# Kernel tuning notes

Measured on AMD Instinct MI355X. Metric: run time of the kernel, lower is better.

The kernel has to match this reference:

```python
import jax, jax.numpy as jnp
import numpy as np

NUM_SEGMENTS = 512
N = 200000
D = 256


def setup_inputs() -> dict:
    key = jax.random.key(0)
    k = jax.random.split(key, 6)
    x = jax.random.normal(k[0], (N, D), dtype=jnp.float32)
    batch = jnp.sort(jax.random.randint(k[1], (N,), 0, NUM_SEGMENTS))
    batch = batch.at[-1].set(NUM_SEGMENTS - 1)  # ensure batch.max()+1 == NUM_SEGMENTS
    W1 = jax.random.normal(k[2], (D, D // 2), dtype=jnp.float32) * (1.0 / np.sqrt(D))
    b1 = jax.random.normal(k[3], (D // 2,), dtype=jnp.float32) * 0.01
    W2 = jax.random.normal(k[4], (D // 2, 1), dtype=jnp.float32) * (1.0 / np.sqrt(D // 2))
    b2 = jax.random.normal(k[5], (1,), dtype=jnp.float32) * 0.01
    return {"x": x, "batch": batch, "W1": W1, "b1": b1, "W2": W2, "b2": b2}


def reference(x, batch, W1, b1, W2, b2):
    # attention MLP: Linear -> Tanh -> Linear -> [N, 1]
    scores = (jnp.tanh(x @ W1 + b1) @ W2 + b2)[:, 0]  # [N]
    # segment softmax (numerically stable): subtract per-segment max
    smax = jax.ops.segment_max(scores, batch, num_segments=NUM_SEGMENTS)  # [G]
    e = jnp.exp(scores - smax[batch])  # [N]
    denom = jax.ops.segment_sum(e, batch, num_segments=NUM_SEGMENTS)  # [G]
    denom = jnp.where(denom > 0, denom, 1.0)  # guard empty segments (original yields zeros)
    w = e / denom[batch]  # [N]
    # weighted sum pooling per segment -> [G, D]
    return jax.ops.segment_sum(x * w[:, None], batch, num_segments=NUM_SEGMENTS)
```

## Files before the change

kernel.cpp:

```cpp
#include <hip/hip_runtime.h>
#include <hip/hip_bf16.h>
#include <math.h>


typedef __attribute__((ext_vector_type(4))) float f32x4;
typedef __attribute__((ext_vector_type(8))) short s16x8;
typedef __attribute__((ext_vector_type(8))) unsigned short u16x8;

#define MFMA16(A, B, C) __builtin_amdgcn_mfma_f32_16x16x32_bf16((A), (B), (C), 0, 0, 0)

#define MAXP 4
#define PPITCH 260

__device__ __forceinline__ unsigned short f2bf_rne(float f) {
    unsigned int u = __float_as_uint(f);
    unsigned int r = u + 0x7FFFu + ((u >> 16) & 1u);
    return (unsigned short)(r >> 16);
}
__device__ __forceinline__ float bf2f(unsigned short h) {
    return __uint_as_float(((unsigned int)h) << 16);
}
__device__ __forceinline__ unsigned fkey(float f) {
    unsigned u = __float_as_uint(f);
    return (u & 0x80000000u) ? ~u : (u | 0x80000000u);
}
__device__ __forceinline__ float funkey(unsigned k) {
    return __uint_as_float((k & 0x80000000u) ? (k ^ 0x80000000u) : ~k);
}

__global__ __launch_bounds__(256)
void prep_w1(const float* __restrict__ W1, unsigned short* __restrict__ bh,
             unsigned short* __restrict__ bl)
{
    for (int idx = blockIdx.x * 256 + threadIdx.x; idx < 128 * 256;
         idx += gridDim.x * 256) {
        int n = idx & 127, k = idx >> 7;
        float f = W1[(size_t)k * 128 + n];
        unsigned short h = f2bf_rne(f);
        bh[(size_t)n * 256 + k] = h;
        bl[(size_t)n * 256 + k] = f2bf_rne(f - bf2f(h));
    }
}

#define LPITCH 40

__global__ __launch_bounds__(256, 3)
void scores_pool(const float* __restrict__ x,
                 const unsigned short* __restrict__ bh,
                 const unsigned short* __restrict__ bl,
                 const float* __restrict__ b1, const float* __restrict__ W2,
                 const float* __restrict__ b2, const int* __restrict__ batch,
                 float* __restrict__ partials, int N)
{
    __shared__ __align__(16) unsigned short Ahi[128 * LPITCH];
    __shared__ __align__(16) unsigned short Alo[128 * LPITCH];
    __shared__ __align__(16) unsigned short Bhi[128 * LPITCH];
    __shared__ __align__(16) unsigned short Blo[128 * LPITCH];
    __shared__ float sscore[128];
    __shared__ int   sseg[128];
    __shared__ float sew[128];
    __shared__ int   pcnt[MAXP];
    __shared__ int   pstart[MAXP + 1];
    __shared__ unsigned pmaxu[MAXP];
    __shared__ float pm[MAXP];
    __shared__ float psum[MAXP];
    __shared__ __align__(16) float4 redp[4][64];

    const int tid  = threadIdx.x;
    const int wave = tid >> 6;
    const int lane = tid & 63;
    const int c    = lane & 15;
    const int q    = lane >> 4;
    const int rowBase = blockIdx.x * 128;

    f32x4 acc[2][8];
#pragma unroll
    for (int mt = 0; mt < 2; ++mt)
#pragma unroll
        for (int nt = 0; nt < 8; ++nt)
            acc[mt][nt] = (f32x4){0.f, 0.f, 0.f, 0.f};

    const int arow  = rowBase + (tid >> 1);
    const int ak16  = (tid & 1) * 16;
    const int nB    = tid & 127;
    const int bk16  = (tid >> 7) * 16;

    f32x4 pa0, pa1, pa2, pa3;
    u16x8 pb0, pb1, pl0, pl1;

    auto loadA = [&](int k0) {
        if (arow < N) {
            const float* p = x + (size_t)arow * 256 + k0 + ak16;
            pa0 = *(const f32x4*)(p);
            pa1 = *(const f32x4*)(p + 4);
            pa2 = *(const f32x4*)(p + 8);
            pa3 = *(const f32x4*)(p + 12);
        } else {
            pa0 = pa1 = pa2 = pa3 = (f32x4){0.f, 0.f, 0.f, 0.f};
        }
    };
    auto loadB = [&](int k0) {
        const size_t base = (size_t)nB * 256 + k0 + bk16;
        pb0 = *(const u16x8*)(bh + base);
        pb1 = *(const u16x8*)(bh + base + 8);
        pl0 = *(const u16x8*)(bl + base);
        pl1 = *(const u16x8*)(bl + base + 8);
    };

    loadA(0);
    loadB(0);

    for (int it = 0; it < 8; ++it) {
        float af[16];
        *(f32x4*)&af[0]  = pa0; *(f32x4*)&af[4]  = pa1;
        *(f32x4*)&af[8]  = pa2; *(f32x4*)&af[12] = pa3;
        unsigned short ah[16], al[16];
#pragma unroll
        for (int j = 0; j < 8; ++j) {
            float a0 = af[2 * j], a1 = af[2 * j + 1];
            __hip_bfloat162 h2 = __float22bfloat162_rn(make_float2(a0, a1));
            ushort2 hu = *(ushort2*)&h2;
            float r0 = a0 - bf2f(hu.x), r1 = a1 - bf2f(hu.y);
            __hip_bfloat162 l2 = __float22bfloat162_rn(make_float2(r0, r1));
            ushort2 lu = *(ushort2*)&l2;
            ah[2 * j] = hu.x; ah[2 * j + 1] = hu.y;
            al[2 * j] = lu.x; al[2 * j + 1] = lu.y;
        }

        __syncthreads();
        {
            const int ar = tid >> 1;
            *(u16x8*)&Ahi[ar * LPITCH + ak16 + 0] = *(u16x8*)&ah[0];
            *(u16x8*)&Ahi[ar * LPITCH + ak16 + 8] = *(u16x8*)&ah[8];
            *(u16x8*)&Alo[ar * LPITCH + ak16 + 0] = *(u16x8*)&al[0];
            *(u16x8*)&Alo[ar * LPITCH + ak16 + 8] = *(u16x8*)&al[8];
            *(u16x8*)&Bhi[nB * LPITCH + bk16 + 0] = pb0;
            *(u16x8*)&Bhi[nB * LPITCH + bk16 + 8] = pb1;
            *(u16x8*)&Blo[nB * LPITCH + bk16 + 0] = pl0;
            *(u16x8*)&Blo[nB * LPITCH + bk16 + 8] = pl1;
        }
        __syncthreads();

        if (it < 7) {
            loadA((it + 1) * 32);
            loadB((it + 1) * 32);
        }

        s16x8 fah[2], fal[2];
#pragma unroll
        for (int mt = 0; mt < 2; ++mt) {
            int m = wave * 32 + mt * 16 + c;
            fah[mt] = *(const s16x8*)&Ahi[m * LPITCH + q * 8];
            fal[mt] = *(const s16x8*)&Alo[m * LPITCH + q * 8];
        }
#pragma unroll
        for (int nt = 0; nt < 8; ++nt) {
            int nr = nt * 16 + c;
            s16x8 fbh = *(const s16x8*)&Bhi[nr * LPITCH + q * 8];
            s16x8 fbl = *(const s16x8*)&Blo[nr * LPITCH + q * 8];
#pragma unroll
            for (int mt = 0; mt < 2; ++mt) {
                acc[mt][nt] = MFMA16(fah[mt], fbh, acc[mt][nt]);
                acc[mt][nt] = MFMA16(fah[mt], fbl, acc[mt][nt]);
                acc[mt][nt] = MFMA16(fal[mt], fbh, acc[mt][nt]);
            }
        }
    }

    float b1v[8], w2v[8];
#pragma unroll
    for (int nt = 0; nt < 8; ++nt) {
        b1v[nt] = b1[nt * 16 + c];
        w2v[nt] = W2[nt * 16 + c];
    }
    const float bias2 = b2[0];

#pragma unroll
    for (int mt = 0; mt < 2; ++mt) {
#pragma unroll
        for (int reg = 0; reg < 4; ++reg) {
            float p = 0.f;
#pragma unroll
            for (int nt = 0; nt < 8; ++nt) {
                float v = acc[mt][nt][reg] + b1v[nt];
                float e = __expf(2.f * v);
                p += (1.f - 2.f / (e + 1.f)) * w2v[nt];
            }
#pragma unroll
            for (int off = 8; off > 0; off >>= 1)
                p += __shfl_xor(p, off, 16);
            if (c == 0)
                sscore[wave * 32 + mt * 16 + q * 4 + reg] = p + bias2;
        }
    }

    const int nrows = min(128, N - rowBase);
    if (tid < MAXP) { pcnt[tid] = 0; pmaxu[tid] = 0u; psum[tid] = 0.f; }
    if (tid < nrows) sseg[tid] = batch[rowBase + tid];
    __syncthreads();

    const int seg0 = sseg[0];
    const int npc  = min(sseg[nrows - 1] - seg0 + 1, MAXP);
    int pp = 0;
    if (tid < nrows) {
        pp = min(sseg[tid] - seg0, MAXP - 1);
        atomicAdd(&pcnt[pp], 1);
        atomicMax(&pmaxu[pp], fkey(sscore[tid]));
    }
    __syncthreads();
    if (tid == 0) {
        int s = 0;
#pragma unroll
        for (int p2 = 0; p2 < MAXP; ++p2) { pstart[p2] = s; s += pcnt[p2]; }
        pstart[MAXP] = s;
    }
    if (tid < MAXP) pm[tid] = funkey(pmaxu[tid]);
    __syncthreads();
    if (tid < nrows) {
        float e = __expf(sscore[tid] - pm[pp]);
        sew[tid] = e;
        atomicAdd(&psum[pp], e);
    }
    __syncthreads();

    const int fgrp  = tid & 63;
    const int rslot = tid >> 6;
    for (int p = 0; p < npc; ++p) {
        const int r0 = pstart[p], r1 = pstart[p + 1];
        if (r0 == r1) continue;
        float4 pacc = make_float4(0.f, 0.f, 0.f, 0.f);
        for (int r = r0 + rslot; r < r1; r += 4) {
            float w = sew[r];
            float4 v = *(const float4*)(x + (size_t)(rowBase + r) * 256 + fgrp * 4);
            pacc.x = fmaf(w, v.x, pacc.x);
            pacc.y = fmaf(w, v.y, pacc.y);
            pacc.z = fmaf(w, v.z, pacc.z);
            pacc.w = fmaf(w, v.w, pacc.w);
        }
        redp[rslot][fgrp] = pacc;
        __syncthreads();
        if (rslot == 0) {
            float4 t0 = redp[0][fgrp], t1 = redp[1][fgrp];
            float4 t2 = redp[2][fgrp], t3 = redp[3][fgrp];
            t0.x += t1.x + t2.x + t3.x;
            t0.y += t1.y + t2.y + t3.y;
            t0.z += t1.z + t2.z + t3.z;
            t0.w += t1.w + t2.w + t3.w;
            float* P = partials + ((size_t)blockIdx.x * MAXP + p) * PPITCH;
            ((float4*)P)[fgrp] = t0;
            if (fgrp == 0) { P[256] = pm[p]; P[257] = psum[p]; }
        }
        __syncthreads();
    }
}

__device__ __forceinline__ int lower_bound_dev(const int* __restrict__ b, int n, int v)
{
    int lo = 0, hi = n;
    while (lo < hi) {
        int mid = (lo + hi) >> 1;
        if (b[mid] < v) lo = mid + 1; else hi = mid;
    }
    return lo;
}

__global__ __launch_bounds__(256)
void combine_kernel(const float* __restrict__ partials, const int* __restrict__ batch,
                    float* __restrict__ out, int N)
{
    const int g = blockIdx.x;
    const int tid = threadIdx.x;
    __shared__ int sse[2];
    __shared__ int sslot[16];
    __shared__ float sm[16], sscale[16];
    __shared__ float sden;

    if (tid < 2) sse[tid] = lower_bound_dev(batch, N, g + tid);
    __syncthreads();
    const int start = sse[0], end = sse[1];
    if (start >= end) {
        out[(size_t)g * 256 + tid] = 0.f;
        return;
    }
    const int b0 = start >> 7, b1 = (end - 1) >> 7;
    const int nb = min(b1 - b0 + 1, 16);

    if (tid < nb) {
        int b = b0 + tid;
        int slot = min(g - batch[b << 7], MAXP - 1);
        sslot[tid] = slot;
        sm[tid] = partials[((size_t)b * MAXP + slot) * PPITCH + 256];
    }
    __syncthreads();
    if (tid == 0) {
        float M = -INFINITY;
        for (int i = 0; i < nb; ++i) M = fmaxf(M, sm[i]);
        float D = 0.f;
        for (int i = 0; i < nb; ++i) {
            float sc = __expf(sm[i] - M);
            sscale[i] = sc;
            D += sc * partials[((size_t)(b0 + i) * MAXP + sslot[i]) * PPITCH + 257];
        }
        sden = (D > 0.f) ? 1.f / D : 0.f;
    }
    __syncthreads();

    float o = 0.f;
    for (int i = 0; i < nb; ++i)
        o += sscale[i] * partials[((size_t)(b0 + i) * MAXP + sslot[i]) * PPITCH + tid];
    out[(size_t)g * 256 + tid] = o * sden;
}

extern "C" void kernel_launch(void* const* d_in, const int* in_sizes, int n_in,
                              void* d_out, int out_size, void* d_ws, size_t ws_size,
                              hipStream_t stream) {
    const float* x     = (const float*)d_in[0];
    const int*   batch = (const int*)  d_in[1];
    const float* W1    = (const float*)d_in[2];
    const float* b1    = (const float*)d_in[3];
    const float* W2    = (const float*)d_in[4];
    const float* b2    = (const float*)d_in[5];
    float* out = (float*)d_out;

    const int N = in_sizes[1];
    const int G = out_size / 256;

    float* partials = (float*)d_ws;

    unsigned short* bh = (unsigned short*)d_out;
    unsigned short* bl = bh + 128 * 256;

    prep_w1<<<64, 256, 0, stream>>>(W1, bh, bl);
    const int mblocks = (N + 127) / 128;
    scores_pool<<<mblocks, 256, 0, stream>>>(x, bh, bl, b1, W2, b2, batch,
                                             partials, N);
    combine_kernel<<<G, 256, 0, stream>>>(partials, batch, out, N);
}
```

Measured before the change: 364.4 us.

## Stage GEMM tiles with direct global-to-LDS loads, double buffering, and XOR swizzle

Replaces the register-staged load/convert/store path with global_load_lds direct copies into double-buffered, XOR-swizzled LDS tiles. Raw fp32 x is now stored in LDS and split into bf16 hi/lo at fragment-read time. This removes register staging and one barrier per iteration and overlaps the next tile's fetch with MFMA work. The cost is more LDS per block, which lowers the occupancy hint from 3 to 2. It also unrolls the pooling accumulation loop.

```diff
diff --git a/kernel.cpp b/kernel.cpp
--- a/kernel.cpp
+++ b/kernel.cpp
@@ -26,6 +26,12 @@
 }
 __device__ __forceinline__ float funkey(unsigned k) {
     return __uint_as_float((k & 0x80000000u) ? (k ^ 0x80000000u) : ~k);
+}
+
+__device__ __forceinline__ void gload_lds16(const void* g, void* l) {
+    __builtin_amdgcn_global_load_lds(
+        (const __attribute__((address_space(1))) void*)g,
+        (__attribute__((address_space(3))) void*)l, 16, 0, 0);
 }
 
 __global__ __launch_bounds__(256)
@@ -42,9 +48,7 @@
     }
 }
 
-#define LPITCH 40
-
-__global__ __launch_bounds__(256, 3)
+__global__ __launch_bounds__(256, 2)
 void scores_pool(const float* __restrict__ x,
                  const unsigned short* __restrict__ bh,
                  const unsigned short* __restrict__ bl,
@@ -52,10 +56,9 @@
                  const float* __restrict__ b2, const int* __restrict__ batch,
                  float* __restrict__ partials, int N)
 {
-    __shared__ __align__(16) unsigned short Ahi[128 * LPITCH];
-    __shared__ __align__(16) unsigned short Alo[128 * LPITCH];
-    __shared__ __align__(16) unsigned short Bhi[128 * LPITCH];
-    __shared__ __align__(16) unsigned short Blo[128 * LPITCH];
+    __shared__ __align__(16) float          ldsA [2][128 * 32];
+    __shared__ __align__(16) unsigned short ldsBh[2][128 * 32];
+    __shared__ __align__(16) unsigned short ldsBl[2][128 * 32];
     __shared__ float sscore[128];
     __shared__ int   sseg[128];
     __shared__ float sew[128];
@@ -80,84 +83,95 @@
         for (int nt = 0; nt < 8; ++nt)
             acc[mt][nt] = (f32x4){0.f, 0.f, 0.f, 0.f};
 
-    const int arow  = rowBase + (tid >> 1);
-    const int ak16  = (tid & 1) * 16;
-    const int nB    = tid & 127;
-    const int bk16  = (tid >> 7) * 16;
-
-    f32x4 pa0, pa1, pa2, pa3;
-    u16x8 pb0, pb1, pl0, pl1;
-
-    auto loadA = [&](int k0) {
-        if (arow < N) {
-            const float* p = x + (size_t)arow * 256 + k0 + ak16;
-            pa0 = *(const f32x4*)(p);
-            pa1 = *(const f32x4*)(p + 4);
-            pa2 = *(const f32x4*)(p + 8);
-            pa3 = *(const f32x4*)(p + 12);
-        } else {
-            pa0 = pa1 = pa2 = pa3 = (f32x4){0.f, 0.f, 0.f, 0.f};
+    size_t aG[4];
+#pragma unroll
+    for (int j = 0; j < 4; ++j) {
+        int r  = (tid >> 3) + 32 * j;
+        int cg = (tid & 7) ^ (r & 7);
+        int grow = min(rowBase + r, N - 1);
+        aG[j] = (size_t)grow * 1024 + (size_t)cg * 16;
+    }
+    size_t bG[2];
+#pragma unroll
+    for (int j = 0; j < 2; ++j) {
+        int r  = (tid >> 2) + 64 * j;
+        int cg = (tid & 3) ^ ((r >> 1) & 3);
+        bG[j] = (size_t)r * 512 + (size_t)cg * 16;
+    }
+
+    int aIdx[2][2];
+#pragma unroll
+    for (int mt = 0; mt < 2; ++mt) {
+        int m = wave * 32 + mt * 16 + c;
+        aIdx[mt][0] = m * 32 + ((2 * q)     ^ (m & 7)) * 4;
+        aIdx[mt][1] = m * 32 + ((2 * q + 1) ^ (m & 7)) * 4;
+    }
+    int bIdx[8];
+#pragma unroll
+    for (int nt = 0; nt < 8; ++nt) {
+        int nr = nt * 16 + c;
+        bIdx[nt] = nr * 32 + (q ^ ((nr >> 1) & 3)) * 8;
+    }
+
+    const char* xB  = (const char*)x;
+    const char* bhB = (const char*)bh;
+    const char* blB = (const char*)bl;
+
+    auto stage = [&](int it, int buf) {
+        char* lA = (char*)&ldsA[buf][0]  + tid * 16;
+        char* lH = (char*)&ldsBh[buf][0] + tid * 16;
+        char* lL = (char*)&ldsBl[buf][0] + tid * 16;
+        const size_t koffA = (size_t)it * 128;
+        const size_t koffB = (size_t)it * 64;
+#pragma unroll
+        for (int j = 0; j < 4; ++j)
+            gload_lds16(xB + aG[j] + koffA, lA + j * 4096);
+#pragma unroll
+        for (int j = 0; j < 2; ++j) {
+            gload_lds16(bhB + bG[j] + koffB, lH + j * 4096);
+            gload_lds16(blB + bG[j] + koffB, lL + j * 4096);
         }
     };
-    auto loadB = [&](int k0) {
-        const size_t base = (size_t)nB * 256 + k0 + bk16;
-        pb0 = *(const u16x8*)(bh + base);
-        pb1 = *(const u16x8*)(bh + base + 8);
-        pl0 = *(const u16x8*)(bl + base);
-        pl1 = *(const u16x8*)(bl + base + 8);
-    };
-
-    loadA(0);
-    loadB(0);
+
+    stage(0, 0);
+    asm volatile("s_waitcnt vmcnt(0)" ::: "memory");
+    __syncthreads();
 
     for (int it = 0; it < 8; ++it) {
-        float af[16];
-        *(f32x4*)&af[0]  = pa0; *(f32x4*)&af[4]  = pa1;
-        *(f32x4*)&af[8]  = pa2; *(f32x4*)&af[12] = pa3;
-        unsigned short ah[16], al[16];
-#pragma unroll
-        for (int j = 0; j < 8; ++j) {
-            float a0 = af[2 * j], a1 = af[2 * j + 1];
-            __hip_bfloat162 h2 = __float22bfloat162_rn(make_float2(a0, a1));
-            ushort2 hu = *(ushort2*)&h2;
-            float r0 = a0 - bf2f(hu.x), r1 = a1 - bf2f(hu.y);
-            __hip_bfloat162 l2 = __float22bfloat162_rn(make_float2(r0, r1));
-            ushort2 lu = *(ushort2*)&l2;
-            ah[2 * j] = hu.x; ah[2 * j + 1] = hu.y;
-            al[2 * j] = lu.x; al[2 * j + 1] = lu.y;
-        }
-
-        __syncthreads();
-        {
-            const int ar = tid >> 1;
-            *(u16x8*)&Ahi[ar * LPITCH + ak16 + 0] = *(u16x8*)&ah[0];
-            *(u16x8*)&Ahi[ar * LPITCH + ak16 + 8] = *(u16x8*)&ah[8];
-            *(u16x8*)&Alo[ar * LPITCH + ak16 + 0] = *(u16x8*)&al[0];
-            *(u16x8*)&Alo[ar * LPITCH + ak16 + 8] = *(u16x8*)&al[8];
-            *(u16x8*)&Bhi[nB * LPITCH + bk16 + 0] = pb0;
-            *(u16x8*)&Bhi[nB * LPITCH + bk16 + 8] = pb1;
-            *(u16x8*)&Blo[nB * LPITCH + bk16 + 0] = pl0;
-            *(u16x8*)&Blo[nB * LPITCH + bk16 + 8] = pl1;
-        }
-        __syncthreads();
-
-        if (it < 7) {
-            loadA((it + 1) * 32);
-            loadB((it + 1) * 32);
-        }
+        const int cur = it & 1;
+        if (it < 7) stage(it + 1, cur ^ 1);
+
+        const float*          Ab = &ldsA[cur][0];
+        const unsigned short* Hb = &ldsBh[cur][0];
+        const unsigned short* Lb = &ldsBl[cur][0];
 
         s16x8 fah[2], fal[2];
 #pragma unroll
         for (int mt = 0; mt < 2; ++mt) {
-            int m = wave * 32 + mt * 16 + c;
-            fah[mt] = *(const s16x8*)&Ahi[m * LPITCH + q * 8];
-            fal[mt] = *(const s16x8*)&Alo[m * LPITCH + q * 8];
-        }
+            f32x4 u = *(const f32x4*)(Ab + aIdx[mt][0]);
+            f32x4 v = *(const f32x4*)(Ab + aIdx[mt][1]);
+            float f[8];
+            *(f32x4*)&f[0] = u; *(f32x4*)&f[4] = v;
+            unsigned short ah[8], al[8];
+#pragma unroll
+            for (int jj = 0; jj < 4; ++jj) {
+                float a0 = f[2 * jj], a1 = f[2 * jj + 1];
+                __hip_bfloat162 h2 = __float22bfloat162_rn(make_float2(a0, a1));
+                ushort2 hu = *(ushort2*)&h2;
+                float r0 = a0 - bf2f(hu.x), r1 = a1 - bf2f(hu.y);
+                __hip_bfloat162 l2 = __float22bfloat162_rn(make_float2(r0, r1));
+                ushort2 lu = *(ushort2*)&l2;
+                ah[2 * jj] = hu.x; ah[2 * jj + 1] = hu.y;
+                al[2 * jj] = lu.x; al[2 * jj + 1] = lu.y;
+            }
+            fah[mt] = *(s16x8*)&ah[0];
+            fal[mt] = *(s16x8*)&al[0];
+        }
+
 #pragma unroll
         for (int nt = 0; nt < 8; ++nt) {
-            int nr = nt * 16 + c;
-            s16x8 fbh = *(const s16x8*)&Bhi[nr * LPITCH + q * 8];
-            s16x8 fbl = *(const s16x8*)&Blo[nr * LPITCH + q * 8];
+            s16x8 fbh = *(const s16x8*)(Hb + bIdx[nt]);
+            s16x8 fbl = *(const s16x8*)(Lb + bIdx[nt]);
 #pragma unroll
             for (int mt = 0; mt < 2; ++mt) {
                 acc[mt][nt] = MFMA16(fah[mt], fbh, acc[mt][nt]);
@@ -165,6 +179,9 @@
                 acc[mt][nt] = MFMA16(fal[mt], fbh, acc[mt][nt]);
             }
         }
+
+        asm volatile("s_waitcnt vmcnt(0)" ::: "memory");
+        __syncthreads();
     }
 
     float b1v[8], w2v[8];
@@ -229,6 +246,7 @@
         const int r0 = pstart[p], r1 = pstart[p + 1];
         if (r0 == r1) continue;
         float4 pacc = make_float4(0.f, 0.f, 0.f, 0.f);
+#pragma unroll 4
         for (int r = r0 + rslot; r < r1; r += 4) {
             float w = sew[r];
             float4 v = *(const float4*)(x + (size_t)(rowBase + r) * 256 + fgrp * 4);
```

After: 349.3 us. 1.04x faster.
